# Kernel tuning notes

Hardware: AMD Instinct MI355X
Metric: run time of the kernel (lower is better)

The kernel has to match this reference:

```python
import jax, jax.numpy as jnp
import numpy as np

B, S, D = 128, 512, 1024
VOCAB = 30524
START_ID = VOCAB - 2  # len(tokenizer) - 2
END_ID = VOCAB - 1


def setup_inputs() -> dict:
    key = jax.random.key(0)
    k_in, k_ids, k_pos, kw1, kb1, kw2, kb2 = jax.random.split(key, 7)
    inputs = jax.random.normal(k_in, (B, S, D), dtype=jnp.float32)
    # random token ids, then plant one START and one END marker per row
    ids = jax.random.randint(k_ids, (B, S), 0, START_ID)
    start_pos = jax.random.randint(k_pos, (B,), 1, S // 2)          # in [1, S/2)
    span_len = jax.random.randint(jax.random.fold_in(k_pos, 1), (B,), 1, 32)
    end_pos = start_pos + span_len + 1                               # < S
    rows = jnp.arange(B)
    ids = ids.at[rows, start_pos].set(START_ID)
    ids = ids.at[rows, end_pos].set(END_ID)
    bound = 1.0 / np.sqrt(D)
    W1 = jax.random.uniform(kw1, (D, D), jnp.float32, -bound, bound)
    b1 = jax.random.uniform(kb1, (D,), jnp.float32, -bound, bound)
    W2 = jax.random.uniform(kw2, (2, D), jnp.float32, -bound, bound)
    b2 = jax.random.uniform(kb2, (2,), jnp.float32, -bound, bound)
    return {"inputs": inputs, "input_ids": ids, "W1": W1, "b1": b1, "W2": W2, "b2": b2}


def reference(inputs, input_ids, W1, b1, W2, b2):
    # span mask: positions strictly between the START and END markers
    start_pos = jnp.argmax(input_ids == START_ID, axis=1)  # [B]
    end_pos = jnp.argmax(input_ids == END_ID, axis=1)      # [B]
    pos = jnp.arange(input_ids.shape[1])                   # [S]
    mask = (pos[None, :] > start_pos[:, None]) & (pos[None, :] < end_pos[:, None])
    # masked gather-sum over the span: euph [B, D]
    euph = jnp.einsum("bs,bsd->bd", mask.astype(inputs.dtype), inputs)
    # linear1 -> dropout(eval=identity) -> linear2
    h = euph @ W1.T + b1
    out = h @ W2.T + b2  # [B, 2]
    return out
```

## Files before the change

### kernel.cpp

```cpp
#include <hip/hip_runtime.h>

#define BB 128
#define SS 512
#define DD 1024
#define START_ID 30522
#define END_ID   30523

__global__ void span_euph_kernel(const float* __restrict__ inputs,
                                 const int* __restrict__ ids,
                                 float* __restrict__ euph,
                                 float* __restrict__ Mbuf) {
    const int b = blockIdx.x;
    const int t = threadIdx.x;

    if (b == 0) {
        for (int i = t; i < 2 * DD; i += 256) Mbuf[i] = 0.0f;
    }

    __shared__ int s_start, s_end;
    for (int s = t; s < SS; s += 256) {
        int id = ids[b * SS + s];
        if (id == START_ID) s_start = s;
        if (id == END_ID)   s_end = s;
    }
    __syncthreads();
    const int st = s_start;
    const int en = s_end;

    float4 acc = make_float4(0.f, 0.f, 0.f, 0.f);
    const size_t rowbase = (size_t)b * SS * DD + 4 * t;
    for (int s = st + 1; s < en; ++s) {
        float4 v = *(const float4*)(inputs + rowbase + (size_t)s * DD);
        acc.x += v.x; acc.y += v.y; acc.z += v.z; acc.w += v.w;
    }
    *(float4*)(euph + (size_t)b * DD + 4 * t) = acc;
}

__global__ void build_M_kernel(const float* __restrict__ W1,
                               const float* __restrict__ W2,
                               float* __restrict__ Mbuf) {
    const int bid = blockIdx.x;
    const int t = threadIdx.x;
    const int k = (bid & 3) * 256 + t;
    const int d0 = (bid >> 2) * 16;

    float m0 = 0.f, m1 = 0.f;
    for (int i = 0; i < 16; ++i) {
        int d = d0 + i;
        float w1 = W1[(size_t)d * DD + k];
        m0 += W2[d]      * w1;
        m1 += W2[DD + d] * w1;
    }
    atomicAdd(&Mbuf[k],      m0);
    atomicAdd(&Mbuf[DD + k], m1);
}

__global__ void out_kernel(const float* __restrict__ euph,
                           const float* __restrict__ Mbuf,
                           const float* __restrict__ W2,
                           const float* __restrict__ b1,
                           const float* __restrict__ b2,
                           float* __restrict__ out) {
    const int b = blockIdx.x;
    const int t = threadIdx.x;

    float s0 = 0.f, s1 = 0.f, c0 = 0.f, c1 = 0.f;
    for (int k = t; k < DD; k += 256) {
        float e = euph[(size_t)b * DD + k];
        s0 += e * Mbuf[k];
        s1 += e * Mbuf[DD + k];
        float bv = b1[k];
        c0 += W2[k]      * bv;
        c1 += W2[DD + k] * bv;
    }

    __shared__ float r0[256], r1[256], r2[256], r3[256];
    r0[t] = s0; r1[t] = s1; r2[t] = c0; r3[t] = c1;
    __syncthreads();
    for (int off = 128; off >= 1; off >>= 1) {
        if (t < off) {
            r0[t] += r0[t + off];
            r1[t] += r1[t + off];
            r2[t] += r2[t + off];
            r3[t] += r3[t + off];
        }
        __syncthreads();
    }
    if (t == 0) {
        out[2 * b]     = r0[0] + r2[0] + b2[0];
        out[2 * b + 1] = r1[0] + r3[0] + b2[1];
    }
}

extern "C" void kernel_launch(void* const* d_in, const int* in_sizes, int n_in,
                              void* d_out, int out_size, void* d_ws, size_t ws_size,
                              hipStream_t stream) {
    const float* inputs = (const float*)d_in[0];
    const int*   ids    = (const int*)d_in[1];
    const float* W1     = (const float*)d_in[2];
    const float* b1     = (const float*)d_in[3];
    const float* W2     = (const float*)d_in[4];
    const float* b2     = (const float*)d_in[5];
    float* out = (float*)d_out;

    float* euph = (float*)d_ws;
    float* Mbuf = euph + (size_t)BB * DD;

    span_euph_kernel<<<BB, 256, 0, stream>>>(inputs, ids, euph, Mbuf);
    build_M_kernel<<<256, 256, 0, stream>>>(W1, W2, Mbuf);
    out_kernel<<<BB, 256, 0, stream>>>(euph, Mbuf, W2, b1, b2, out);
}
```

Measured before the change: 321.8 us.

## Fuse span sum with output projection and replace atomics with partial sums

Cuts the three-kernel pipeline down to two. A prep kernel writes 64 partial slices of M = W2·W1 with float4 loads, which removes the atomicAdds and the zeroing of Mbuf, and it precomputes the bias constants once. A row kernel then sums the span, reduces the partial M slices and takes the dot product in the same block. This removes the euph round trip and one launch, but every row block now re-reads the full 512 KB of partials.

```diff
diff --git a/kernel.cpp b/kernel.cpp
--- a/kernel.cpp
+++ b/kernel.cpp
@@ -5,21 +5,66 @@
 #define DD 1024
 #define START_ID 30522
 #define END_ID   30523
+#define NPART 64
 
-__global__ void span_euph_kernel(const float* __restrict__ inputs,
-                                 const int* __restrict__ ids,
-                                 float* __restrict__ euph,
-                                 float* __restrict__ Mbuf) {
+__device__ __forceinline__ void f4add(float4& a, const float4 b, float s) {
+    a.x += s * b.x; a.y += s * b.y; a.z += s * b.z; a.w += s * b.w;
+}
+
+__global__ void prep_kernel(const float* __restrict__ W1,
+                            const float* __restrict__ W2,
+                            const float* __restrict__ b1,
+                            const float* __restrict__ b2,
+                            float* __restrict__ Mpart,
+                            float* __restrict__ consts) {
+    const int p = blockIdx.x;
+    const int t = threadIdx.x;
+
+    if (p < NPART) {
+        const int k4 = 4 * t;
+        float4 m0 = make_float4(0.f, 0.f, 0.f, 0.f);
+        float4 m1 = make_float4(0.f, 0.f, 0.f, 0.f);
+        #pragma unroll
+        for (int i = 0; i < 16; ++i) {
+            const int d = p * 16 + i;
+            const float4 w1 = *(const float4*)(W1 + (size_t)d * DD + k4);
+            f4add(m0, w1, W2[d]);
+            f4add(m1, w1, W2[DD + d]);
+        }
+        *(float4*)(Mpart + (size_t)p * 2 * DD + k4) = m0;
+        *(float4*)(Mpart + (size_t)p * 2 * DD + DD + k4) = m1;
+    } else {
+        float c0 = 0.f, c1 = 0.f;
+        for (int k = t; k < DD; k += 256) {
+            const float bv = b1[k];
+            c0 += W2[k]      * bv;
+            c1 += W2[DD + k] * bv;
+        }
+        __shared__ float r0[256], r1[256];
+        r0[t] = c0; r1[t] = c1;
+        __syncthreads();
+        for (int off = 128; off >= 1; off >>= 1) {
+            if (t < off) { r0[t] += r0[t + off]; r1[t] += r1[t + off]; }
+            __syncthreads();
+        }
+        if (t == 0) {
+            consts[0] = r0[0] + b2[0];
+            consts[1] = r1[0] + b2[1];
+        }
+    }
+}
+
+__global__ void row_kernel(const float* __restrict__ inputs,
+                           const int* __restrict__ ids,
+                           const float* __restrict__ Mpart,
+                           const float* __restrict__ consts,
+                           float* __restrict__ out) {
     const int b = blockIdx.x;
     const int t = threadIdx.x;
 
-    if (b == 0) {
-        for (int i = t; i < 2 * DD; i += 256) Mbuf[i] = 0.0f;
-    }
-
     __shared__ int s_start, s_end;
     for (int s = t; s < SS; s += 256) {
-        int id = ids[b * SS + s];
+        const int id = ids[b * SS + s];
         if (id == START_ID) s_start = s;
         if (id == END_ID)   s_end = s;
     }
@@ -30,65 +75,34 @@
     float4 acc = make_float4(0.f, 0.f, 0.f, 0.f);
     const size_t rowbase = (size_t)b * SS * DD + 4 * t;
     for (int s = st + 1; s < en; ++s) {
-        float4 v = *(const float4*)(inputs + rowbase + (size_t)s * DD);
+        const float4 v = *(const float4*)(inputs + rowbase + (size_t)s * DD);
         acc.x += v.x; acc.y += v.y; acc.z += v.z; acc.w += v.w;
     }
-    *(float4*)(euph + (size_t)b * DD + 4 * t) = acc;
-}
 
-__global__ void build_M_kernel(const float* __restrict__ W1,
-                               const float* __restrict__ W2,
-                               float* __restrict__ Mbuf) {
-    const int bid = blockIdx.x;
-    const int t = threadIdx.x;
-    const int k = (bid & 3) * 256 + t;
-    const int d0 = (bid >> 2) * 16;
-
-    float m0 = 0.f, m1 = 0.f;
-    for (int i = 0; i < 16; ++i) {
-        int d = d0 + i;
-        float w1 = W1[(size_t)d * DD + k];
-        m0 += W2[d]      * w1;
-        m1 += W2[DD + d] * w1;
-    }
-    atomicAdd(&Mbuf[k],      m0);
-    atomicAdd(&Mbuf[DD + k], m1);
-}
-
-__global__ void out_kernel(const float* __restrict__ euph,
-                           const float* __restrict__ Mbuf,
-                           const float* __restrict__ W2,
-                           const float* __restrict__ b1,
-                           const float* __restrict__ b2,
-                           float* __restrict__ out) {
-    const int b = blockIdx.x;
-    const int t = threadIdx.x;
-
-    float s0 = 0.f, s1 = 0.f, c0 = 0.f, c1 = 0.f;
-    for (int k = t; k < DD; k += 256) {
-        float e = euph[(size_t)b * DD + k];
-        s0 += e * Mbuf[k];
-        s1 += e * Mbuf[DD + k];
-        float bv = b1[k];
-        c0 += W2[k]      * bv;
-        c1 += W2[DD + k] * bv;
+    float4 M0 = make_float4(0.f, 0.f, 0.f, 0.f);
+    float4 M1 = make_float4(0.f, 0.f, 0.f, 0.f);
+    const float* mp = Mpart + 4 * t;
+    #pragma unroll 8
+    for (int p = 0; p < NPART; ++p) {
+        const float4 a = *(const float4*)(mp + (size_t)p * 2 * DD);
+        const float4 c = *(const float4*)(mp + (size_t)p * 2 * DD + DD);
+        M0.x += a.x; M0.y += a.y; M0.z += a.z; M0.w += a.w;
+        M1.x += c.x; M1.y += c.y; M1.z += c.z; M1.w += c.w;
     }
 
-    __shared__ float r0[256], r1[256], r2[256], r3[256];
-    r0[t] = s0; r1[t] = s1; r2[t] = c0; r3[t] = c1;
+    float s0 = acc.x * M0.x + acc.y * M0.y + acc.z * M0.z + acc.w * M0.w;
+    float s1 = acc.x * M1.x + acc.y * M1.y + acc.z * M1.z + acc.w * M1.w;
+
+    __shared__ float r0[256], r1[256];
+    r0[t] = s0; r1[t] = s1;
     __syncthreads();
     for (int off = 128; off >= 1; off >>= 1) {
-        if (t < off) {
-            r0[t] += r0[t + off];
-            r1[t] += r1[t + off];
-            r2[t] += r2[t + off];
-            r3[t] += r3[t + off];
-        }
+        if (t < off) { r0[t] += r0[t + off]; r1[t] += r1[t + off]; }
         __syncthreads();
     }
     if (t == 0) {
-        out[2 * b]     = r0[0] + r2[0] + b2[0];
-        out[2 * b + 1] = r1[0] + r3[0] + b2[1];
+        out[2 * b]     = r0[0] + consts[0];
+        out[2 * b + 1] = r1[0] + consts[1];
     }
 }
 
@@ -103,10 +117,9 @@
     const float* b2     = (const float*)d_in[5];
     float* out = (float*)d_out;
 
-    float* euph = (float*)d_ws;
-    float* Mbuf = euph + (size_t)BB * DD;
+    float* Mpart  = (float*)d_ws;
+    float* consts = Mpart + (size_t)NPART * 2 * DD;
 
-    span_euph_kernel<<<BB, 256, 0, stream>>>(inputs, ids, euph, Mbuf);
-    build_M_kernel<<<256, 256, 0, stream>>>(W1, W2, Mbuf);
-    out_kernel<<<BB, 256, 0, stream>>>(euph, Mbuf, W2, b1, b2, out);
+    prep_kernel<<<NPART + 1, 256, 0, stream>>>(W1, W2, b1, b2, Mpart, consts);
+    row_kernel<<<BB, 256, 0, stream>>>(inputs, ids, Mpart, consts, out);
 }
```

Measured after the change: 323.0 us. Within noise of the previous version (+0.4%).
